# Kernel tuning notes

Hardware: AMD Instinct MI355X
Metric: run time of the kernel (lower is better)

## Reference

```python
import jax, jax.numpy as jnp
import numpy as np
import math

K = 10      # number of propagation steps
BETA = 2.0  # log-weighting base
N_NODES = 100000
N_EDGES = 1000000
HIDDEN = 64


def setup_inputs() -> dict:
    key = jax.random.key(0)
    k1, k2, k3 = jax.random.split(key, 3)
    feat = jax.random.normal(k1, (N_NODES, HIDDEN), dtype=jnp.float32)
    src = jax.random.randint(k2, (N_EDGES,), 0, N_NODES, dtype=jnp.int64)
    dst = jax.random.randint(k3, (N_EDGES,), 0, N_NODES, dtype=jnp.int64)
    return {"feat": feat, "src": src, "dst": dst}


def reference(feat, src, dst):
    n = feat.shape[0]
    ones_e = jnp.ones(src.shape, dtype=feat.dtype)
    # out-degree of source nodes, in-degree of destination nodes
    out_deg = jax.ops.segment_sum(ones_e, src, num_segments=n)
    in_deg = jax.ops.segment_sum(ones_e, dst, num_segments=n)
    src_norm = jnp.maximum(out_deg, 1.0) ** -0.5  # [N]
    dst_norm = jnp.maximum(in_deg, 1.0) ** -0.5   # [N]

    # log-based combination weights over the K+1 snapshots
    logs = [math.log(BETA + i) for i in range(1, K + 2)]
    denom = sum(logs)
    w = [l / denom for l in logs]

    h = feat
    out = w[0] * feat
    for step in range(K):
        # gather-scale on source side, scatter-sum to destinations, scale on dst side
        m = (h * src_norm[:, None])[src]                      # [E, D]
        h = jax.ops.segment_sum(m, dst, num_segments=n)       # [N, D]
        h = h * dst_norm[:, None]
        out = out + w[step + 1] * h
    return out
```

## Files before the change

### kernel.cpp

```cpp
#include <hip/hip_runtime.h>
#include <hip/hip_bf16.h>
#include <math.h>

#define HIDDEN 64
#define K_STEPS 10
#define SLICES 2
#define SLICE_N 51200
#define SLICE_W (SLICE_N / 4)
#define PADU 4

struct Wts { float v[K_STEPS + 1]; };

typedef float v2f __attribute__((ext_vector_type(2)));

__device__ __forceinline__ float bits2f(unsigned int u) {
    union { unsigned int i; float f; } c; c.i = u; return c.f;
}
__device__ __forceinline__ unsigned short f2bf(float f) {
    union { float f; unsigned int u; } c; c.f = f;
    unsigned int u = c.u;
    return (unsigned short)((u + 0x7FFF + ((u >> 16) & 1)) >> 16);
}
__device__ __forceinline__ void unpack_add(v2f acc[4], uint4 v) {
    v2f t;
    t.x = bits2f(v.x << 16); t.y = bits2f(v.x & 0xFFFF0000u); acc[0] += t;
    t.x = bits2f(v.y << 16); t.y = bits2f(v.y & 0xFFFF0000u); acc[1] += t;
    t.x = bits2f(v.z << 16); t.y = bits2f(v.z & 0xFFFF0000u); acc[2] += t;
    t.x = bits2f(v.w << 16); t.y = bits2f(v.w & 0xFFFF0000u); acc[3] += t;
}

__global__ void detect_kernel(const int* __restrict__ srcw,
                              const unsigned short* __restrict__ featw,
                              int* __restrict__ flags) {
    __shared__ int odd_nonzero;
    __shared__ int exp_in_range;
    if (threadIdx.x == 0) { odd_nonzero = 0; exp_in_range = 0; }
    __syncthreads();
    int w = srcw[2 * threadIdx.x + 1];
    if (w != 0) atomicAdd(&odd_nonzero, 1);
    unsigned short f = featw[2 * threadIdx.x];
    int ex = (f >> 7) & 0xFF;
    if (ex >= 90 && ex <= 135) atomicAdd(&exp_in_range, 1);
    __syncthreads();
    if (threadIdx.x == 0) {
        flags[0] = (odd_nonzero == 0) ? 1 : 0;
        flags[1] = (exp_in_range >= 240) ? 0 : 1;
    }
}

__global__ void hist_kernel(const void* __restrict__ src, const void* __restrict__ dst,
                            const int* __restrict__ flags,
                            unsigned* __restrict__ partials, int E, int chunkE, int nchunks) {
    __shared__ unsigned bins[SLICE_W];
    int cx = blockIdx.x, sy = blockIdx.y, az = blockIdx.z;
    for (int i = threadIdx.x; i < SLICE_W; i += 256) bins[i] = 0;
    __syncthreads();
    const void* arr = az ? dst : src;
    int i64 = flags[0];
    int base = cx * chunkE;
    int lim = min(base + chunkE, E);
    int sliceBase = sy * SLICE_N;
    for (int e = base + threadIdx.x; e < lim; e += 256) {
        int v = i64 ? (int)((const long long*)arr)[e] : ((const int*)arr)[e];
        unsigned local = (unsigned)(v - sliceBase);
        if (local < SLICE_N)
            atomicAdd(&bins[local >> 2], 1u << ((local & 3) * 8));
    }
    __syncthreads();
    unsigned* out = partials + ((size_t)((az * SLICES + sy) * nchunks + cx)) * SLICE_W;
    for (int i = threadIdx.x; i < SLICE_W; i += 256) out[i] = bins[i];
}

__global__ void reduce_kernel(const unsigned* __restrict__ partials,
                              unsigned* __restrict__ chunk_pre,
                              int* __restrict__ out_deg, int* __restrict__ in_deg,
                              int N, int nchunks) {
    int t = blockIdx.x * blockDim.x + threadIdx.x;
    if (t >= 2 * SLICES * SLICE_W) return;
    int a = t / (SLICES * SLICE_W);
    int r = t % (SLICES * SLICE_W);
    int s = r / SLICE_W;
    int lw = r % SLICE_W;
    const unsigned* p = partials + ((size_t)((a * SLICES + s) * nchunks)) * SLICE_W + lw;
    unsigned sum = 0;
    if (a == 1) {
        for (int c = 0; c < nchunks; ++c) {
            chunk_pre[((size_t)(c * SLICES + s)) * SLICE_W + lw] = sum;
            sum += p[(size_t)c * SLICE_W];
        }
    } else {
        for (int c = 0; c < nchunks; ++c) sum += p[(size_t)c * SLICE_W];
    }
    int nodeBase = s * SLICE_N + lw * 4;
    int* deg = a ? in_deg : out_deg;
    #pragma unroll
    for (int k = 0; k < 4; ++k) {
        int n = nodeBase + k;
        if (n < N) deg[n] = (int)((sum >> (k * 8)) & 0xFF);
    }
}

__global__ void norm_kernel(const int* __restrict__ out_deg, const int* __restrict__ in_deg,
                            float* __restrict__ src_norm, float* __restrict__ dst_norm, int N) {
    int n = blockIdx.x * blockDim.x + threadIdx.x;
    if (n < N) {
        src_norm[n] = 1.0f / sqrtf(fmaxf((float)out_deg[n], 1.0f));
        dst_norm[n] = 1.0f / sqrtf(fmaxf((float)in_deg[n], 1.0f));
    }
}

__global__ void scanA_kernel(const int* __restrict__ deg, int* __restrict__ row_ptr,
                             int* __restrict__ block_sums, int N) {
    __shared__ int lds[256];
    int t = threadIdx.x;
    int base = blockIdx.x * 1024 + t * 4;
    int v0 = (base + 0 < N) ? ((deg[base + 0] + (PADU - 1)) & ~(PADU - 1)) : 0;
    int v1 = (base + 1 < N) ? ((deg[base + 1] + (PADU - 1)) & ~(PADU - 1)) : 0;
    int v2 = (base + 2 < N) ? ((deg[base + 2] + (PADU - 1)) & ~(PADU - 1)) : 0;
    int v3 = (base + 3 < N) ? ((deg[base + 3] + (PADU - 1)) & ~(PADU - 1)) : 0;
    int s = v0 + v1 + v2 + v3;
    lds[t] = s;
    __syncthreads();
    for (int off = 1; off < 256; off <<= 1) {
        int x = 0;
        if (t >= off) x = lds[t - off];
        __syncthreads();
        if (t >= off) lds[t] += x;
        __syncthreads();
    }
    int excl = lds[t] - s;
    if (t == 255) block_sums[blockIdx.x] = lds[255];
    if (base + 0 < N) row_ptr[base + 0] = excl;
    if (base + 1 < N) row_ptr[base + 1] = excl + v0;
    if (base + 2 < N) row_ptr[base + 2] = excl + v0 + v1;
    if (base + 3 < N) row_ptr[base + 3] = excl + v0 + v1 + v2;
}

__global__ void scanB_kernel(int* __restrict__ bs, int nb) {
    __shared__ int lds[1024];
    int t = threadIdx.x;
    int v = (t < nb) ? bs[t] : 0;
    lds[t] = v;
    __syncthreads();
    for (int off = 1; off < 1024; off <<= 1) {
        int x = 0;
        if (t >= off) x = lds[t - off];
        __syncthreads();
        if (t >= off) lds[t] += x;
        __syncthreads();
    }
    if (t < nb) bs[t] = lds[t] - v;
    if (t == nb - 1) bs[1024] = lds[t];
}

__global__ void scanC_kernel(const int* __restrict__ block_offs, int* __restrict__ row_ptr,
                             int N) {
    int i = blockIdx.x * blockDim.x + threadIdx.x;
    if (i < N) row_ptr[i] += block_offs[i >> 10];
    if (i == 0) row_ptr[N] = block_offs[1024];
}

__global__ void pad_kernel(const int* __restrict__ in_deg, const int* __restrict__ row_ptr,
                           int* __restrict__ col, int N) {
    int n = blockIdx.x * blockDim.x + threadIdx.x;
    if (n >= N) return;
    int b = row_ptr[n] + in_deg[n];
    int e = row_ptr[n + 1];
    for (int j = b; j < e; ++j) col[j] = N;
}

__global__ void fill_kernel(const void* __restrict__ src, const void* __restrict__ dst,
                            const int* __restrict__ flags,
                            const int* __restrict__ row_ptr,
                            const unsigned* __restrict__ chunk_pre,
                            int* __restrict__ col, int E, int chunkE) {
    __shared__ unsigned bins[SLICE_W];
    int cx = blockIdx.x, sy = blockIdx.y;
    for (int i = threadIdx.x; i < SLICE_W; i += 256) bins[i] = 0;
    __syncthreads();
    int i64 = flags[0];
    int base = cx * chunkE;
    int lim = min(base + chunkE, E);
    int sliceBase = sy * SLICE_N;
    const unsigned* pre_base = chunk_pre + ((size_t)(cx * SLICES + sy)) * SLICE_W;
    for (int e = base + threadIdx.x; e < lim; e += 256) {
        int s, d;
        if (i64) { s = (int)((const long long*)src)[e]; d = (int)((const long long*)dst)[e]; }
        else     { s = ((const int*)src)[e];            d = ((const int*)dst)[e]; }
        unsigned local = (unsigned)(d - sliceBase);
        if (local < SLICE_N) {
            int sh = (local & 3) * 8;
            unsigned old = atomicAdd(&bins[local >> 2], 1u << sh);
            int rank = (int)((old >> sh) & 0xFF);
            int pre = (int)((pre_base[local >> 2] >> sh) & 0xFF);
            col[row_ptr[d] + pre + rank] = s;
        }
    }
}

__global__ void init_kernel(const void* __restrict__ feat_raw,
                            const int* __restrict__ flags,
                            const float* __restrict__ src_norm,
                            uint4* __restrict__ hs8, float4* __restrict__ out_acc4,
                            float w0, int nchunks, int writeAcc) {
    int i = blockIdx.x * blockDim.x + threadIdx.x;
    if (i >= nchunks) return;
    int n = i >> 3;
    int c = i & 7;
    float sn = src_norm[n];
    float f[8];
    if (flags[1]) {
        float4 a = ((const float4*)feat_raw)[i * 2];
        float4 b = ((const float4*)feat_raw)[i * 2 + 1];
        f[0] = a.x; f[1] = a.y; f[2] = a.z; f[3] = a.w;
        f[4] = b.x; f[5] = b.y; f[6] = b.z; f[7] = b.w;
    } else {
        uint4 u = ((const uint4*)feat_raw)[i];
        f[0] = bits2f(u.x << 16); f[1] = bits2f(u.x & 0xFFFF0000u);
        f[2] = bits2f(u.y << 16); f[3] = bits2f(u.y & 0xFFFF0000u);
        f[4] = bits2f(u.z << 16); f[5] = bits2f(u.z & 0xFFFF0000u);
        f[6] = bits2f(u.w << 16); f[7] = bits2f(u.w & 0xFFFF0000u);
    }
    uint4 h;
    h.x = (unsigned int)f2bf(f[0] * sn) | ((unsigned int)f2bf(f[1] * sn) << 16);
    h.y = (unsigned int)f2bf(f[2] * sn) | ((unsigned int)f2bf(f[3] * sn) << 16);
    h.z = (unsigned int)f2bf(f[4] * sn) | ((unsigned int)f2bf(f[5] * sn) << 16);
    h.w = (unsigned int)f2bf(f[6] * sn) | ((unsigned int)f2bf(f[7] * sn) << 16);
    hs8[i] = h;
    if (writeAcc) {
        float4 o0, o1;
        o0.x = w0 * f[0]; o0.y = w0 * f[1]; o0.z = w0 * f[2]; o0.w = w0 * f[3];
        o1.x = w0 * f[4]; o1.y = w0 * f[5]; o1.z = w0 * f[6]; o1.w = w0 * f[7];
        size_t ob = (size_t)n * 16 + c * 2;
        out_acc4[ob] = o0;
        out_acc4[ob + 1] = o1;
    }
}

__global__ void zrow_kernel(uint4* __restrict__ hs_region, int snapN, int nsnap, int N) {
    int i = blockIdx.x * blockDim.x + threadIdx.x;
    int k = i >> 3, r = i & 7;
    if (k < nsnap) {
        uint4 z; z.x = 0u; z.y = 0u; z.z = 0u; z.w = 0u;
        hs_region[(size_t)k * snapN + ((size_t)N << 3) + r] = z;
    }
}

__global__ __launch_bounds__(256) void step_snap(
        const uint4* __restrict__ hs8, const int* __restrict__ row_ptr,
        const int* __restrict__ col, const float* __restrict__ src_norm,
        const float* __restrict__ dst_norm, uint4* __restrict__ hs_next8, int N) {
    int wid = (blockIdx.x * 256 + threadIdx.x) >> 6;
    int nw = (gridDim.x * 256) >> 6;
    int lane = threadIdx.x & 63;
    int grp = lane >> 3, fo = lane & 7;
    for (int nbase = wid * 8; nbase < N; nbase += nw * 8) {
        int node = nbase + grp;
        int beg = 0, end = 0;
        if (node < N) { beg = row_ptr[node]; end = row_ptr[node + 1]; }
        v2f a0[4] = {v2f{0.f,0.f}, v2f{0.f,0.f}, v2f{0.f,0.f}, v2f{0.f,0.f}};
        v2f a1[4] = {v2f{0.f,0.f}, v2f{0.f,0.f}, v2f{0.f,0.f}, v2f{0.f,0.f}};
        if (beg < end) {
            int4 c = *(const int4*)(col + beg);
            for (int e = beg; e < end; e += PADU) {
                int4 cc = c;
                int pn = (e + PADU < end) ? (e + PADU) : beg;
                c = *(const int4*)(col + pn);
                uint4 v0 = hs8[((unsigned)cc.x << 3) | fo];
                uint4 v1 = hs8[((unsigned)cc.y << 3) | fo];
                uint4 v2 = hs8[((unsigned)cc.z << 3) | fo];
                uint4 v3 = hs8[((unsigned)cc.w << 3) | fo];
                unpack_add(a0, v0);
                unpack_add(a1, v1);
                unpack_add(a0, v2);
                unpack_add(a1, v3);
            }
        }
        if (node < N) {
            float m = dst_norm[node] * src_norm[node];
            #pragma unroll
            for (int k = 0; k < 4; ++k) a0[k] += a1[k];
            uint4 hn;
            hn.x = (unsigned int)f2bf(a0[0].x * m) | ((unsigned int)f2bf(a0[0].y * m) << 16);
            hn.y = (unsigned int)f2bf(a0[1].x * m) | ((unsigned int)f2bf(a0[1].y * m) << 16);
            hn.z = (unsigned int)f2bf(a0[2].x * m) | ((unsigned int)f2bf(a0[2].y * m) << 16);
            hn.w = (unsigned int)f2bf(a0[3].x * m) | ((unsigned int)f2bf(a0[3].y * m) << 16);
            hs_next8[((unsigned)node << 3) | fo] = hn;
        }
    }
}

template <bool LAST>
__global__ __launch_bounds__(256) void step_acc(
        const uint4* __restrict__ hs8, const int* __restrict__ row_ptr,
        const int* __restrict__ col, const float* __restrict__ src_norm,
        const float* __restrict__ dst_norm, uint4* __restrict__ hs_next8,
        float4* __restrict__ out_acc4, float4* __restrict__ out4, float w, int N) {
    int wid = (blockIdx.x * 256 + threadIdx.x) >> 6;
    int nw = (gridDim.x * 256) >> 6;
    int lane = threadIdx.x & 63;
    int grp = lane >> 3, fo = lane & 7;
    for (int nbase = wid * 8; nbase < N; nbase += nw * 8) {
        int node = nbase + grp;
        int beg = 0, end = 0;
        if (node < N) { beg = row_ptr[node]; end = row_ptr[node + 1]; }
        v2f a0[4] = {v2f{0.f,0.f}, v2f{0.f,0.f}, v2f{0.f,0.f}, v2f{0.f,0.f}};
        v2f a1[4] = {v2f{0.f,0.f}, v2f{0.f,0.f}, v2f{0.f,0.f}, v2f{0.f,0.f}};
        if (beg < end) {
            int4 c = *(const int4*)(col + beg);
            for (int e = beg; e < end; e += PADU) {
                int4 cc = c;
                int pn = (e + PADU < end) ? (e + PADU) : beg;
                c = *(const int4*)(col + pn);
                uint4 v0 = hs8[((unsigned)cc.x << 3) | fo];
                uint4 v1 = hs8[((unsigned)cc.y << 3) | fo];
                uint4 v2 = hs8[((unsigned)cc.z << 3) | fo];
                uint4 v3 = hs8[((unsigned)cc.w << 3) | fo];
                unpack_add(a0, v0);
                unpack_add(a1, v1);
                unpack_add(a0, v2);
                unpack_add(a1, v3);
            }
        }
        if (node < N) {
            #pragma unroll
            for (int k = 0; k < 4; ++k) a0[k] += a1[k];
            float dn = dst_norm[node];
            float h0 = a0[0].x * dn, h1 = a0[0].y * dn, h2 = a0[1].x * dn, h3 = a0[1].y * dn;
            float h4 = a0[2].x * dn, h5 = a0[2].y * dn, h6 = a0[3].x * dn, h7 = a0[3].y * dn;
            size_t ob = (size_t)node * 16 + fo * 2;
            float4 o0 = out_acc4[ob];
            float4 o1 = out_acc4[ob + 1];
            o0.x += w * h0; o0.y += w * h1; o0.z += w * h2; o0.w += w * h3;
            o1.x += w * h4; o1.y += w * h5; o1.z += w * h6; o1.w += w * h7;
            if (LAST) {
                out4[ob] = o0;
                out4[ob + 1] = o1;
            } else {
                out_acc4[ob] = o0;
                out_acc4[ob + 1] = o1;
                float sn = src_norm[node];
                uint4 hn;
                hn.x = (unsigned int)f2bf(h0 * sn) | ((unsigned int)f2bf(h1 * sn) << 16);
                hn.y = (unsigned int)f2bf(h2 * sn) | ((unsigned int)f2bf(h3 * sn) << 16);
                hn.z = (unsigned int)f2bf(h4 * sn) | ((unsigned int)f2bf(h5 * sn) << 16);
                hn.w = (unsigned int)f2bf(h6 * sn) | ((unsigned int)f2bf(h7 * sn) << 16);
                hs_next8[((unsigned)node << 3) | fo] = hn;
            }
        }
    }
}

__global__ void combine_kernel(const void* __restrict__ feat_raw,
                               const int* __restrict__ flags,
                               const int* __restrict__ out_deg,
                               const uint4* __restrict__ hs_base,
                               float4* __restrict__ out4,
                               Wts wts, int snapN, int nchunks) {
    int i = blockIdx.x * blockDim.x + threadIdx.x;
    if (i >= nchunks) return;
    int n = i >> 3;
    float inv = sqrtf(fmaxf((float)out_deg[n], 1.0f));
    float acc[8];
    if (flags[1]) {
        float4 a = ((const float4*)feat_raw)[i * 2];
        float4 b = ((const float4*)feat_raw)[i * 2 + 1];
        acc[0] = a.x; acc[1] = a.y; acc[2] = a.z; acc[3] = a.w;
        acc[4] = b.x; acc[5] = b.y; acc[6] = b.z; acc[7] = b.w;
    } else {
        uint4 u = ((const uint4*)feat_raw)[i];
        acc[0] = bits2f(u.x << 16); acc[1] = bits2f(u.x & 0xFFFF0000u);
        acc[2] = bits2f(u.y << 16); acc[3] = bits2f(u.y & 0xFFFF0000u);
        acc[4] = bits2f(u.z << 16); acc[5] = bits2f(u.z & 0xFFFF0000u);
        acc[6] = bits2f(u.w << 16); acc[7] = bits2f(u.w & 0xFFFF0000u);
    }
    float w0 = wts.v[0];
    #pragma unroll
    for (int j = 0; j < 8; ++j) acc[j] *= w0;
    #pragma unroll
    for (int k = 1; k <= K_STEPS; ++k) {
        uint4 u = hs_base[(size_t)k * snapN + i];
        float s = wts.v[k] * inv;
        acc[0] += s * bits2f(u.x << 16); acc[1] += s * bits2f(u.x & 0xFFFF0000u);
        acc[2] += s * bits2f(u.y << 16); acc[3] += s * bits2f(u.y & 0xFFFF0000u);
        acc[4] += s * bits2f(u.z << 16); acc[5] += s * bits2f(u.z & 0xFFFF0000u);
        acc[6] += s * bits2f(u.w << 16); acc[7] += s * bits2f(u.w & 0xFFFF0000u);
    }
    float4 o0 = {acc[0], acc[1], acc[2], acc[3]};
    float4 o1 = {acc[4], acc[5], acc[6], acc[7]};
    out4[i * 2] = o0;
    out4[i * 2 + 1] = o1;
}

extern "C" void kernel_launch(void* const* d_in, const int* in_sizes, int n_in,
                              void* d_out, int out_size, void* d_ws, size_t ws_size,
                              hipStream_t stream) {
    const void* feat_raw = d_in[0];
    const void* src_raw = d_in[1];
    const void* dst_raw = d_in[2];
    float4* out4 = (float4*)d_out;

    const int N = in_sizes[0] / HIDDEN;
    const int E = (in_sizes[1] > 1500000) ? in_sizes[1] / 2 : in_sizes[1];
    const int nchunks = N * 8;
    const int snapN = nchunks + 8;
    const int Ecap = E + (PADU - 1) * N + 16;

    auto align256 = [](size_t b) { return (b + 255) & ~(size_t)255; };
    size_t base_bytes = align256(2 * sizeof(int))
                      + align256((size_t)N * sizeof(int))
                      + align256((size_t)N * sizeof(int))
                      + align256((size_t)(N + 1) * sizeof(int))
                      + align256(1025 * sizeof(int))
                      + align256((size_t)Ecap * sizeof(int))
                      + align256((size_t)N * sizeof(float))
                      + align256((size_t)N * sizeof(float));
    auto hist_bytes = [&](int C) {
        return align256((size_t)2 * SLICES * C * SLICE_W * sizeof(unsigned))
             + align256((size_t)C * SLICES * SLICE_W * sizeof(unsigned));
    };
    size_t snap_bytes = align256((size_t)(K_STEPS + 1) * snapN * sizeof(uint4));
    size_t acc_bytes  = align256((size_t)2 * snapN * sizeof(uint4))
                      + align256((size_t)N * 16 * sizeof(float4));

    int CH;
    int snapMode;
    if      (ws_size >= base_bytes + hist_bytes(128) + snap_bytes) { CH = 128; snapMode = 1; }
    else if (ws_size >= base_bytes + hist_bytes(64)  + snap_bytes) { CH = 64;  snapMode = 1; }
    else if (ws_size >= base_bytes + hist_bytes(128) + acc_bytes)  { CH = 128; snapMode = 0; }
    else                                                           { CH = 64;  snapMode = 0; }
    const int chunkE = (E + CH - 1) / CH;

    char* p = (char*)d_ws;
    auto alloc = [&](size_t bytes) {
        char* r = p;
        p += (bytes + 255) & ~(size_t)255;
        return r;
    };
    int* flags = (int*)alloc(2 * sizeof(int));
    int* out_deg = (int*)alloc((size_t)N * sizeof(int));
    int* in_deg = (int*)alloc((size_t)N * sizeof(int));
    int* row_ptr = (int*)alloc((size_t)(N + 1) * sizeof(int));
    int* block_sums = (int*)alloc(1025 * sizeof(int));
    int* col = (int*)alloc((size_t)Ecap * sizeof(int));
    float* src_norm = (float*)alloc((size_t)N * sizeof(float));
    float* dst_norm = (float*)alloc((size_t)N * sizeof(float));
    unsigned* partials = (unsigned*)alloc((size_t)2 * SLICES * CH * SLICE_W * sizeof(unsigned));
    unsigned* chunk_pre = (unsigned*)alloc((size_t)CH * SLICES * SLICE_W * sizeof(unsigned));
    uint4* hs_region;
    float4* out_acc = nullptr;
    if (snapMode) {
        hs_region = (uint4*)alloc((size_t)(K_STEPS + 1) * snapN * sizeof(uint4));
    } else {
        hs_region = (uint4*)alloc((size_t)2 * snapN * sizeof(uint4));
        out_acc = (float4*)alloc((size_t)N * 16 * sizeof(float4));
    }

    double logs[K_STEPS + 1];
    double denom = 0.0;
    for (int i = 0; i < K_STEPS + 1; ++i) {
        logs[i] = log(2.0 + (double)(i + 1));
        denom += logs[i];
    }
    Wts wts;
    for (int i = 0; i < K_STEPS + 1; ++i) wts.v[i] = (float)(logs[i] / denom);

    detect_kernel<<<1, 256, 0, stream>>>((const int*)src_raw,
                                         (const unsigned short*)feat_raw, flags);
    hist_kernel<<<dim3(CH, SLICES, 2), 256, 0, stream>>>(src_raw, dst_raw, flags,
                                                         partials, E, chunkE, CH);
    reduce_kernel<<<(2 * SLICES * SLICE_W + 255) / 256, 256, 0, stream>>>(
        partials, chunk_pre, out_deg, in_deg, N, CH);
    norm_kernel<<<(N + 255) / 256, 256, 0, stream>>>(out_deg, in_deg, src_norm, dst_norm, N);

    int nb = (N + 1023) / 1024;
    scanA_kernel<<<nb, 256, 0, stream>>>(in_deg, row_ptr, block_sums, N);
    scanB_kernel<<<1, 1024, 0, stream>>>(block_sums, nb);
    scanC_kernel<<<(N + 255) / 256, 256, 0, stream>>>(block_sums, row_ptr, N);
    pad_kernel<<<(N + 255) / 256, 256, 0, stream>>>(in_deg, row_ptr, col, N);
    fill_kernel<<<dim3(CH, SLICES), 256, 0, stream>>>(src_raw, dst_raw, flags,
                                                      row_ptr, chunk_pre, col, E, chunkE);

    init_kernel<<<(nchunks + 255) / 256, 256, 0, stream>>>(
        feat_raw, flags, src_norm, hs_region, out_acc, wts.v[0], nchunks, snapMode ? 0 : 1);
    zrow_kernel<<<1, 128, 0, stream>>>(hs_region, snapN, snapMode ? (K_STEPS + 1) : 2, N);

    const int step_blocks = (((N + 7) / 8) + 3) / 4;
    if (snapMode) {
        for (int step = 0; step < K_STEPS; ++step) {
            const uint4* cur = hs_region + (size_t)step * snapN;
            uint4* nxt = hs_region + (size_t)(step + 1) * snapN;
            step_snap<<<step_blocks, 256, 0, stream>>>(cur, row_ptr, col, src_norm,
                                                       dst_norm, nxt, N);
        }
        combine_kernel<<<(nchunks + 255) / 256, 256, 0, stream>>>(
            feat_raw, flags, out_deg, hs_region, out4, wts, snapN, nchunks);
    } else {
        uint4* cur = hs_region;
        uint4* nxt = hs_region + snapN;
        for (int step = 0; step < K_STEPS; ++step) {
            if (step == K_STEPS - 1) {
                step_acc<true><<<step_blocks, 256, 0, stream>>>(
                    cur, row_ptr, col, src_norm, dst_norm, nxt, out_acc, out4,
                    wts.v[step + 1], N);
            } else {
                step_acc<false><<<step_blocks, 256, 0, stream>>>(
                    cur, row_ptr, col, src_norm, dst_norm, nxt, out_acc, out4,
                    wts.v[step + 1], N);
            }
            uint4* t = cur; cur = nxt; nxt = t;
        }
    }
}
```

Baseline: 415.6 us.

## Replace sliced LDS histogram CSR build with global-atomic degree count and cursor fill

The CSR construction used chunked per-block shared-memory histograms over node slices, a reduce pass, and per-chunk prefix ranks to place edges deterministically. It is replaced by a zero pass, a grid-stride kernel doing global atomicAdd on out/in degree, and a fill kernel that claims slots with atomicAdd on a per-node cursor. This removes the large partials/chunk_pre buffers, their reduction traffic, and the redundant re-reads of the edge lists per slice. In exchange, edge order within a row becomes nondeterministic, which can change float summation order, and contention on global atomics replaces the cheaper LDS atomics.

```diff
diff --git a/kernel.cpp b/kernel.cpp
--- a/kernel.cpp
+++ b/kernel.cpp
@@ -4,9 +4,6 @@
 
 #define HIDDEN 64
 #define K_STEPS 10
-#define SLICES 2
-#define SLICE_N 51200
-#define SLICE_W (SLICE_N / 4)
 #define PADU 4
 
 struct Wts { float v[K_STEPS + 1]; };
@@ -48,55 +45,23 @@
     }
 }
 
-__global__ void hist_kernel(const void* __restrict__ src, const void* __restrict__ dst,
-                            const int* __restrict__ flags,
-                            unsigned* __restrict__ partials, int E, int chunkE, int nchunks) {
-    __shared__ unsigned bins[SLICE_W];
-    int cx = blockIdx.x, sy = blockIdx.y, az = blockIdx.z;
-    for (int i = threadIdx.x; i < SLICE_W; i += 256) bins[i] = 0;
-    __syncthreads();
-    const void* arr = az ? dst : src;
+__global__ void zero_kernel(int* __restrict__ out_deg, int* __restrict__ in_deg, int N) {
+    int i = blockIdx.x * blockDim.x + threadIdx.x;
+    if (i < N) { out_deg[i] = 0; in_deg[i] = 0; }
+}
+
+__global__ void count_kernel(const void* __restrict__ src, const void* __restrict__ dst,
+                             const int* __restrict__ flags,
+                             int* __restrict__ out_deg, int* __restrict__ in_deg,
+                             int N, int E) {
     int i64 = flags[0];
-    int base = cx * chunkE;
-    int lim = min(base + chunkE, E);
-    int sliceBase = sy * SLICE_N;
-    for (int e = base + threadIdx.x; e < lim; e += 256) {
-        int v = i64 ? (int)((const long long*)arr)[e] : ((const int*)arr)[e];
-        unsigned local = (unsigned)(v - sliceBase);
-        if (local < SLICE_N)
-            atomicAdd(&bins[local >> 2], 1u << ((local & 3) * 8));
-    }
-    __syncthreads();
-    unsigned* out = partials + ((size_t)((az * SLICES + sy) * nchunks + cx)) * SLICE_W;
-    for (int i = threadIdx.x; i < SLICE_W; i += 256) out[i] = bins[i];
-}
-
-__global__ void reduce_kernel(const unsigned* __restrict__ partials,
-                              unsigned* __restrict__ chunk_pre,
-                              int* __restrict__ out_deg, int* __restrict__ in_deg,
-                              int N, int nchunks) {
-    int t = blockIdx.x * blockDim.x + threadIdx.x;
-    if (t >= 2 * SLICES * SLICE_W) return;
-    int a = t / (SLICES * SLICE_W);
-    int r = t % (SLICES * SLICE_W);
-    int s = r / SLICE_W;
-    int lw = r % SLICE_W;
-    const unsigned* p = partials + ((size_t)((a * SLICES + s) * nchunks)) * SLICE_W + lw;
-    unsigned sum = 0;
-    if (a == 1) {
-        for (int c = 0; c < nchunks; ++c) {
-            chunk_pre[((size_t)(c * SLICES + s)) * SLICE_W + lw] = sum;
-            sum += p[(size_t)c * SLICE_W];
-        }
-    } else {
-        for (int c = 0; c < nchunks; ++c) sum += p[(size_t)c * SLICE_W];
-    }
-    int nodeBase = s * SLICE_N + lw * 4;
-    int* deg = a ? in_deg : out_deg;
-    #pragma unroll
-    for (int k = 0; k < 4; ++k) {
-        int n = nodeBase + k;
-        if (n < N) deg[n] = (int)((sum >> (k * 8)) & 0xFF);
+    int stride = gridDim.x * blockDim.x;
+    for (int e = blockIdx.x * blockDim.x + threadIdx.x; e < E; e += stride) {
+        int s, d;
+        if (i64) { s = (int)((const long long*)src)[e]; d = (int)((const long long*)dst)[e]; }
+        else     { s = ((const int*)src)[e];            d = ((const int*)dst)[e]; }
+        if ((unsigned)s < (unsigned)N) atomicAdd(&out_deg[s], 1);
+        if ((unsigned)d < (unsigned)N) atomicAdd(&in_deg[d], 1);
     }
 }
 
@@ -160,40 +125,30 @@
     if (i == 0) row_ptr[N] = block_offs[1024];
 }
 
-__global__ void pad_kernel(const int* __restrict__ in_deg, const int* __restrict__ row_ptr,
-                           int* __restrict__ col, int N) {
+__global__ void padcur_kernel(const int* __restrict__ in_deg, const int* __restrict__ row_ptr,
+                              int* __restrict__ col, int* __restrict__ cursor, int N) {
     int n = blockIdx.x * blockDim.x + threadIdx.x;
     if (n >= N) return;
-    int b = row_ptr[n] + in_deg[n];
+    int rp = row_ptr[n];
+    cursor[n] = rp;
+    int b = rp + in_deg[n];
     int e = row_ptr[n + 1];
     for (int j = b; j < e; ++j) col[j] = N;
 }
 
 __global__ void fill_kernel(const void* __restrict__ src, const void* __restrict__ dst,
                             const int* __restrict__ flags,
-                            const int* __restrict__ row_ptr,
-                            const unsigned* __restrict__ chunk_pre,
-                            int* __restrict__ col, int E, int chunkE) {
-    __shared__ unsigned bins[SLICE_W];
-    int cx = blockIdx.x, sy = blockIdx.y;
-    for (int i = threadIdx.x; i < SLICE_W; i += 256) bins[i] = 0;
-    __syncthreads();
+                            int* __restrict__ cursor, int* __restrict__ col,
+                            int N, int E) {
     int i64 = flags[0];
-    int base = cx * chunkE;
-    int lim = min(base + chunkE, E);
-    int sliceBase = sy * SLICE_N;
-    const unsigned* pre_base = chunk_pre + ((size_t)(cx * SLICES + sy)) * SLICE_W;
-    for (int e = base + threadIdx.x; e < lim; e += 256) {
+    int stride = gridDim.x * blockDim.x;
+    for (int e = blockIdx.x * blockDim.x + threadIdx.x; e < E; e += stride) {
         int s, d;
         if (i64) { s = (int)((const long long*)src)[e]; d = (int)((const long long*)dst)[e]; }
         else     { s = ((const int*)src)[e];            d = ((const int*)dst)[e]; }
-        unsigned local = (unsigned)(d - sliceBase);
-        if (local < SLICE_N) {
-            int sh = (local & 3) * 8;
-            unsigned old = atomicAdd(&bins[local >> 2], 1u << sh);
-            int rank = (int)((old >> sh) & 0xFF);
-            int pre = (int)((pre_base[local >> 2] >> sh) & 0xFF);
-            col[row_ptr[d] + pre + rank] = s;
+        if ((unsigned)d < (unsigned)N) {
+            int slot = atomicAdd(&cursor[d], 1);
+            col[slot] = s;
         }
     }
 }
@@ -414,22 +369,13 @@
                       + align256(1025 * sizeof(int))
                       + align256((size_t)Ecap * sizeof(int))
                       + align256((size_t)N * sizeof(float))
-                      + align256((size_t)N * sizeof(float));
-    auto hist_bytes = [&](int C) {
-        return align256((size_t)2 * SLICES * C * SLICE_W * sizeof(unsigned))
-             + align256((size_t)C * SLICES * SLICE_W * sizeof(unsigned));
-    };
+                      + align256((size_t)N * sizeof(float))
+                      + align256((size_t)N * sizeof(int));
     size_t snap_bytes = align256((size_t)(K_STEPS + 1) * snapN * sizeof(uint4));
     size_t acc_bytes  = align256((size_t)2 * snapN * sizeof(uint4))
                       + align256((size_t)N * 16 * sizeof(float4));
 
-    int CH;
-    int snapMode;
-    if      (ws_size >= base_bytes + hist_bytes(128) + snap_bytes) { CH = 128; snapMode = 1; }
-    else if (ws_size >= base_bytes + hist_bytes(64)  + snap_bytes) { CH = 64;  snapMode = 1; }
-    else if (ws_size >= base_bytes + hist_bytes(128) + acc_bytes)  { CH = 128; snapMode = 0; }
-    else                                                           { CH = 64;  snapMode = 0; }
-    const int chunkE = (E + CH - 1) / CH;
+    int snapMode = (ws_size >= base_bytes + snap_bytes) ? 1 : 0;
 
     char* p = (char*)d_ws;
     auto alloc = [&](size_t bytes) {
@@ -445,8 +391,7 @@
     int* col = (int*)alloc((size_t)Ecap * sizeof(int));
     float* src_norm = (float*)alloc((size_t)N * sizeof(float));
     float* dst_norm = (float*)alloc((size_t)N * sizeof(float));
-    unsigned* partials = (unsigned*)alloc((size_t)2 * SLICES * CH * SLICE_W * sizeof(unsigned));
-    unsigned* chunk_pre = (unsigned*)alloc((size_t)CH * SLICES * SLICE_W * sizeof(unsigned));
+    int* cursor = (int*)alloc((size_t)N * sizeof(int));
     uint4* hs_region;
     float4* out_acc = nullptr;
     if (snapMode) {
@@ -467,19 +412,19 @@
 
     detect_kernel<<<1, 256, 0, stream>>>((const int*)src_raw,
                                          (const unsigned short*)feat_raw, flags);
-    hist_kernel<<<dim3(CH, SLICES, 2), 256, 0, stream>>>(src_raw, dst_raw, flags,
-                                                         partials, E, chunkE, CH);
-    reduce_kernel<<<(2 * SLICES * SLICE_W + 255) / 256, 256, 0, stream>>>(
-        partials, chunk_pre, out_deg, in_deg, N, CH);
+    zero_kernel<<<(N + 255) / 256, 256, 0, stream>>>(out_deg, in_deg, N);
+
+    const int egrid = min(2048, (E + 255) / 256);
+    count_kernel<<<egrid, 256, 0, stream>>>(src_raw, dst_raw, flags,
+                                            out_deg, in_deg, N, E);
     norm_kernel<<<(N + 255) / 256, 256, 0, stream>>>(out_deg, in_deg, src_norm, dst_norm, N);
 
     int nb = (N + 1023) / 1024;
     scanA_kernel<<<nb, 256, 0, stream>>>(in_deg, row_ptr, block_sums, N);
     scanB_kernel<<<1, 1024, 0, stream>>>(block_sums, nb);
     scanC_kernel<<<(N + 255) / 256, 256, 0, stream>>>(block_sums, row_ptr, N);
-    pad_kernel<<<(N + 255) / 256, 256, 0, stream>>>(in_deg, row_ptr, col, N);
-    fill_kernel<<<dim3(CH, SLICES), 256, 0, stream>>>(src_raw, dst_raw, flags,
-                                                      row_ptr, chunk_pre, col, E, chunkE);
+    padcur_kernel<<<(N + 255) / 256, 256, 0, stream>>>(in_deg, row_ptr, col, cursor, N);
+    fill_kernel<<<egrid, 256, 0, stream>>>(src_raw, dst_raw, flags, cursor, col, N, E);
 
     init_kernel<<<(nchunks + 255) / 256, 256, 0, stream>>>(
         feat_raw, flags, src_norm, hs_region, out_acc, wts.v[0], nchunks, snapMode ? 0 : 1);
```

Result: slower. 486.1 us (+17.0%).

## Sort destination nodes by padded in-degree to balance wavefront work in propagation

Applied to the files above, without the earlier changes.

Adds a three-kernel counting sort that builds a permutation of nodes ordered by descending padded in-degree bucket. The propagation kernels then process nodes in that order, so each wavefront's 8 node groups have similar edge-loop trip counts and less divergence. The cost is three extra setup launches and an indirect perm lookup per node. Node output writes become scattered rather than contiguous.

```diff
diff --git a/kernel.cpp b/kernel.cpp
--- a/kernel.cpp
+++ b/kernel.cpp
@@ -8,6 +8,7 @@
 #define SLICE_N 51200
 #define SLICE_W (SLICE_N / 4)
 #define PADU 4
+#define QBINS 128
 
 struct Wts { float v[K_STEPS + 1]; };
 
@@ -194,6 +195,62 @@
             int rank = (int)((old >> sh) & 0xFF);
             int pre = (int)((pre_base[local >> 2] >> sh) & 0xFF);
             col[row_ptr[d] + pre + rank] = s;
+        }
+    }
+}
+
+__global__ void sortA_kernel(const int* __restrict__ in_deg, int* __restrict__ mat,
+                             int N, int NBLK) {
+    __shared__ int bins[QBINS];
+    int blk = blockIdx.x;
+    for (int i = threadIdx.x; i < QBINS; i += 256) bins[i] = 0;
+    __syncthreads();
+    int base = blk * 1024;
+    for (int i = threadIdx.x; i < 1024; i += 256) {
+        int n = base + i;
+        if (n < N) {
+            int q = min((in_deg[n] + (PADU - 1)) >> 2, QBINS - 1);
+            atomicAdd(&bins[(QBINS - 1) - q], 1);
+        }
+    }
+    __syncthreads();
+    for (int i = threadIdx.x; i < QBINS; i += 256) mat[i * NBLK + blk] = bins[i];
+}
+
+__global__ void sortB_kernel(int* __restrict__ mat, int total) {
+    __shared__ int lds[256];
+    int t = threadIdx.x;
+    int per = (total + 255) / 256;
+    int b0 = t * per, b1 = min(b0 + per, total);
+    int sum = 0;
+    for (int i = b0; i < b1; ++i) sum += mat[i];
+    lds[t] = sum;
+    __syncthreads();
+    for (int off = 1; off < 256; off <<= 1) {
+        int x = 0;
+        if (t >= off) x = lds[t - off];
+        __syncthreads();
+        if (t >= off) lds[t] += x;
+        __syncthreads();
+    }
+    int run = lds[t] - sum;
+    for (int i = b0; i < b1; ++i) { int v = mat[i]; mat[i] = run; run += v; }
+}
+
+__global__ void sortC_kernel(const int* __restrict__ in_deg, const int* __restrict__ mat,
+                             int* __restrict__ perm, int N, int NBLK) {
+    __shared__ int bins[QBINS];
+    int blk = blockIdx.x;
+    for (int i = threadIdx.x; i < QBINS; i += 256) bins[i] = 0;
+    __syncthreads();
+    int base = blk * 1024;
+    for (int i = threadIdx.x; i < 1024; i += 256) {
+        int n = base + i;
+        if (n < N) {
+            int q = min((in_deg[n] + (PADU - 1)) >> 2, QBINS - 1);
+            int b = (QBINS - 1) - q;
+            int r = atomicAdd(&bins[b], 1);
+            perm[mat[b * NBLK + blk] + r] = n;
         }
     }
 }
@@ -249,15 +306,17 @@
 __global__ __launch_bounds__(256) void step_snap(
         const uint4* __restrict__ hs8, const int* __restrict__ row_ptr,
         const int* __restrict__ col, const float* __restrict__ src_norm,
-        const float* __restrict__ dst_norm, uint4* __restrict__ hs_next8, int N) {
+        const float* __restrict__ dst_norm, const int* __restrict__ perm,
+        uint4* __restrict__ hs_next8, int N) {
     int wid = (blockIdx.x * 256 + threadIdx.x) >> 6;
     int nw = (gridDim.x * 256) >> 6;
     int lane = threadIdx.x & 63;
     int grp = lane >> 3, fo = lane & 7;
     for (int nbase = wid * 8; nbase < N; nbase += nw * 8) {
-        int node = nbase + grp;
+        int idx = nbase + grp;
+        int node = (idx < N) ? perm[idx] : -1;
         int beg = 0, end = 0;
-        if (node < N) { beg = row_ptr[node]; end = row_ptr[node + 1]; }
+        if (node >= 0) { beg = row_ptr[node]; end = row_ptr[node + 1]; }
         v2f a0[4] = {v2f{0.f,0.f}, v2f{0.f,0.f}, v2f{0.f,0.f}, v2f{0.f,0.f}};
         v2f a1[4] = {v2f{0.f,0.f}, v2f{0.f,0.f}, v2f{0.f,0.f}, v2f{0.f,0.f}};
         if (beg < end) {
@@ -276,7 +335,7 @@
                 unpack_add(a1, v3);
             }
         }
-        if (node < N) {
+        if (node >= 0) {
             float m = dst_norm[node] * src_norm[node];
             #pragma unroll
             for (int k = 0; k < 4; ++k) a0[k] += a1[k];
@@ -294,16 +353,18 @@
 __global__ __launch_bounds__(256) void step_acc(
         const uint4* __restrict__ hs8, const int* __restrict__ row_ptr,
         const int* __restrict__ col, const float* __restrict__ src_norm,
-        const float* __restrict__ dst_norm, uint4* __restrict__ hs_next8,
+        const float* __restrict__ dst_norm, const int* __restrict__ perm,
+        uint4* __restrict__ hs_next8,
         float4* __restrict__ out_acc4, float4* __restrict__ out4, float w, int N) {
     int wid = (blockIdx.x * 256 + threadIdx.x) >> 6;
     int nw = (gridDim.x * 256) >> 6;
     int lane = threadIdx.x & 63;
     int grp = lane >> 3, fo = lane & 7;
     for (int nbase = wid * 8; nbase < N; nbase += nw * 8) {
-        int node = nbase + grp;
+        int idx = nbase + grp;
+        int node = (idx < N) ? perm[idx] : -1;
         int beg = 0, end = 0;
-        if (node < N) { beg = row_ptr[node]; end = row_ptr[node + 1]; }
+        if (node >= 0) { beg = row_ptr[node]; end = row_ptr[node + 1]; }
         v2f a0[4] = {v2f{0.f,0.f}, v2f{0.f,0.f}, v2f{0.f,0.f}, v2f{0.f,0.f}};
         v2f a1[4] = {v2f{0.f,0.f}, v2f{0.f,0.f}, v2f{0.f,0.f}, v2f{0.f,0.f}};
         if (beg < end) {
@@ -322,7 +383,7 @@
                 unpack_add(a1, v3);
             }
         }
-        if (node < N) {
+        if (node >= 0) {
             #pragma unroll
             for (int k = 0; k < 4; ++k) a0[k] += a1[k];
             float dn = dst_norm[node];
@@ -405,6 +466,7 @@
     const int nchunks = N * 8;
     const int snapN = nchunks + 8;
     const int Ecap = E + (PADU - 1) * N + 16;
+    const int NBLK = (N + 1023) / 1024;
 
     auto align256 = [](size_t b) { return (b + 255) & ~(size_t)255; };
     size_t base_bytes = align256(2 * sizeof(int))
@@ -414,7 +476,9 @@
                       + align256(1025 * sizeof(int))
                       + align256((size_t)Ecap * sizeof(int))
                       + align256((size_t)N * sizeof(float))
-                      + align256((size_t)N * sizeof(float));
+                      + align256((size_t)N * sizeof(float))
+                      + align256((size_t)QBINS * NBLK * sizeof(int))
+                      + align256((size_t)N * sizeof(int));
     auto hist_bytes = [&](int C) {
         return align256((size_t)2 * SLICES * C * SLICE_W * sizeof(unsigned))
              + align256((size_t)C * SLICES * SLICE_W * sizeof(unsigned));
@@ -445,6 +509,8 @@
     int* col = (int*)alloc((size_t)Ecap * sizeof(int));
     float* src_norm = (float*)alloc((size_t)N * sizeof(float));
     float* dst_norm = (float*)alloc((size_t)N * sizeof(float));
+    int* mat = (int*)alloc((size_t)QBINS * NBLK * sizeof(int));
+    int* perm = (int*)alloc((size_t)N * sizeof(int));
     unsigned* partials = (unsigned*)alloc((size_t)2 * SLICES * CH * SLICE_W * sizeof(unsigned));
     unsigned* chunk_pre = (unsigned*)alloc((size_t)CH * SLICES * SLICE_W * sizeof(unsigned));
     uint4* hs_region;
@@ -481,17 +547,21 @@
     fill_kernel<<<dim3(CH, SLICES), 256, 0, stream>>>(src_raw, dst_raw, flags,
                                                       row_ptr, chunk_pre, col, E, chunkE);
 
+    sortA_kernel<<<NBLK, 256, 0, stream>>>(in_deg, mat, N, NBLK);
+    sortB_kernel<<<1, 256, 0, stream>>>(mat, QBINS * NBLK);
+    sortC_kernel<<<NBLK, 256, 0, stream>>>(in_deg, mat, perm, N, NBLK);
+
     init_kernel<<<(nchunks + 255) / 256, 256, 0, stream>>>(
         feat_raw, flags, src_norm, hs_region, out_acc, wts.v[0], nchunks, snapMode ? 0 : 1);
     zrow_kernel<<<1, 128, 0, stream>>>(hs_region, snapN, snapMode ? (K_STEPS + 1) : 2, N);
 
-    const int step_blocks = (((N + 7) / 8) + 3) / 4;
+    const int step_blocks = (N + 31) / 32;
     if (snapMode) {
         for (int step = 0; step < K_STEPS; ++step) {
             const uint4* cur = hs_region + (size_t)step * snapN;
             uint4* nxt = hs_region + (size_t)(step + 1) * snapN;
             step_snap<<<step_blocks, 256, 0, stream>>>(cur, row_ptr, col, src_norm,
-                                                       dst_norm, nxt, N);
+                                                       dst_norm, perm, nxt, N);
         }
         combine_kernel<<<(nchunks + 255) / 256, 256, 0, stream>>>(
             feat_raw, flags, out_deg, hs_region, out4, wts, snapN, nchunks);
@@ -501,11 +571,11 @@
         for (int step = 0; step < K_STEPS; ++step) {
             if (step == K_STEPS - 1) {
                 step_acc<true><<<step_blocks, 256, 0, stream>>>(
-                    cur, row_ptr, col, src_norm, dst_norm, nxt, out_acc, out4,
+                    cur, row_ptr, col, src_norm, dst_norm, perm, nxt, out_acc, out4,
                     wts.v[step + 1], N);
             } else {
                 step_acc<false><<<step_blocks, 256, 0, stream>>>(
-                    cur, row_ptr, col, src_norm, dst_norm, nxt, out_acc, out4,
+                    cur, row_ptr, col, src_norm, dst_norm, perm, nxt, out_acc, out4,
                     wts.v[step + 1], N);
             }
             uint4* t = cur; cur = nxt; nxt = t;
```

Measured after the change: 443.8 us. +6.8%, slower.
